# Optimization experiments

Hardware: AMD Instinct MI355X
Metric: run time of the kernel (lower is better)

The kernel has to match this reference:

```python
import jax, jax.numpy as jnp
import numpy as np

D, H, DH = 768, 12, 64
W = 256            # one-sided window (attention_window=512 total)
EPS = 1e-6
NEG = -1e9


def layer_norm(x, g, b):
    m = jnp.mean(x, axis=-1, keepdims=True)
    v = jnp.mean((x - m) ** 2, axis=-1, keepdims=True)
    return g * (x - m) * jax.lax.rsqrt(v + EPS) + b


def _blocks3(t, nb):
    # t: [B,H,nb,W,dh] -> keys/values of 3 neighboring blocks [B,H,nb,3W,dh]
    tp = jnp.pad(t, ((0, 0), (0, 0), (1, 1), (0, 0), (0, 0)))
    return jnp.concatenate([tp[:, :, :nb], tp[:, :, 1:nb + 1], tp[:, :, 2:nb + 2]], axis=3)


def sliding_window_attention(x, kpm, Wq, bq, Wk, bk, Wv, bv, Wo, bo):
    B, S, _ = x.shape
    nb = S // W
    def proj(Wm, bm):
        return (x @ Wm + bm).reshape(B, S, H, DH).transpose(0, 2, 1, 3).reshape(B, H, nb, W, DH)
    q = proj(Wq, bq) * (1.0 / np.sqrt(DH))
    k = proj(Wk, bk)
    v = proj(Wv, bv)
    k3 = _blocks3(k, nb)
    v3 = _blocks3(v, nb)
    # scores over local band: [B,H,nb,W,3W]
    s = jnp.einsum('bhnqd,bhnkd->bhnqk', q, k3)
    qi = jnp.arange(W)[:, None]
    kj = jnp.arange(3 * W)[None, :]
    band = jnp.abs(kj - W - qi) <= W                     # [W,3W]
    kg = (jnp.arange(nb)[:, None, None] - 1) * W + kj[None]  # global key idx [nb,1,3W]
    inrange = (kg >= 0) & (kg < S)
    # key padding mask gathered into block layout: [B,nb,3W]
    kpm_b = jnp.pad(kpm.reshape(B, nb, W), ((0, 0), (1, 1), (0, 0)), constant_values=True)
    kpm3 = jnp.concatenate([kpm_b[:, :nb], kpm_b[:, 1:nb + 1], kpm_b[:, 2:nb + 2]], axis=2)
    m = band[None, None, None] & inrange[None, None] & (~kpm3)[:, None, :, None, :]
    s = jnp.where(m, s, NEG)
    p = jax.nn.softmax(s, axis=-1)
    o = jnp.einsum('bhnqk,bhnkd->bhnqd', p, v3)
    o = o.reshape(B, H, S, DH).transpose(0, 2, 1, 3).reshape(B, S, D)
    return o @ Wo + bo


def setup_inputs() -> dict:
    key = jax.random.key(0)
    ks = jax.random.split(key, 12)
    B, S, DF = 2, 4096, 3072
    sc = 1.0 / np.sqrt(D)
    return {
        'x': jax.random.normal(ks[0], (B, S, D), jnp.float32),
        'mask': jnp.zeros((B, S), bool),
        'id': 0,
        'Wq': jax.random.normal(ks[1], (D, D), jnp.float32) * sc,
        'bq': jnp.zeros((D,), jnp.float32),
        'Wk': jax.random.normal(ks[2], (D, D), jnp.float32) * sc,
        'bk': jnp.zeros((D,), jnp.float32),
        'Wv': jax.random.normal(ks[3], (D, D), jnp.float32) * sc,
        'bv': jnp.zeros((D,), jnp.float32),
        'Wo': jax.random.normal(ks[4], (D, D), jnp.float32) * sc,
        'bo': jnp.zeros((D,), jnp.float32),
        'ln1_g': jnp.ones((D,), jnp.float32),
        'ln1_b': jnp.zeros((D,), jnp.float32),
        'W1': jax.random.normal(ks[5], (D, DF), jnp.float32) * sc,
        'b1': jnp.zeros((DF,), jnp.float32),
        'W2': jax.random.normal(ks[6], (DF, D), jnp.float32) * (1.0 / np.sqrt(DF)),
        'b2': jnp.zeros((D,), jnp.float32),
        'ln2_g': jnp.ones((D,), jnp.float32),
        'ln2_b': jnp.zeros((D,), jnp.float32),
    }


def reference(x, mask, id, Wq, bq, Wk, bk, Wv, bv, Wo, bo, ln1_g, ln1_b, W1, b1, W2, b2, ln2_g, ln2_b):
    # Sublayer 1: pre-norm residual around sliding-window self-attention
    h = layer_norm(x, ln1_g, ln1_b)
    x = x + sliding_window_attention(h, mask, Wq, bq, Wk, bk, Wv, bv, Wo, bo)
    # Sublayer 2: pre-norm residual around positionwise FFN
    h = layer_norm(x, ln2_g, ln2_b)
    x = x + (jax.nn.relu(h @ W1 + b1) @ W2 + b2)
    return x
```

## Files before the change

kernel.cpp:

```cpp
#include <hip/hip_runtime.h>
#include <hip/hip_bf16.h>
#include <cstddef>

typedef __attribute__((ext_vector_type(8))) short short8;
typedef __attribute__((ext_vector_type(4))) float f32x4;
typedef __attribute__((ext_vector_type(4))) unsigned short us4;

typedef __attribute__((address_space(1))) void as1_void;
typedef __attribute__((address_space(3))) void as3_void;

__device__ __forceinline__ void gload16(const void* g, void* lds) {
  __builtin_amdgcn_global_load_lds((as1_void*)(void*)g, (as3_void*)lds, 16, 0, 0);
}

__device__ inline unsigned short f2bf(float f) {
  union { float f; unsigned int u; } v; v.f = f;
  return (unsigned short)((v.u + 0x7FFFu + ((v.u >> 16) & 1u)) >> 16);
}

__device__ __forceinline__ float exp2v(float x) {
  float r; asm("v_exp_f32 %0, %1" : "=v"(r) : "v"(x)); return r;
}
__device__ __forceinline__ unsigned cvtpk(float a, float b) {
  unsigned r; asm("v_cvt_pk_bf16_f32 %0, %1, %2" : "=v"(r) : "v"(a), "v"(b)); return r;
}

__global__ __launch_bounds__(256) void ln_kernel(const float* __restrict__ x,
    const float* __restrict__ g, const float* __restrict__ b,
    unsigned short* __restrict__ out)
{
  int row = blockIdx.x, t = threadIdx.x;
  const float* xr = x + (size_t)row * 768;
  float v0 = xr[t], v1 = xr[t + 256], v2 = xr[t + 512];
  float s = v0 + v1 + v2;
  #pragma unroll
  for (int o = 32; o > 0; o >>= 1) s += __shfl_xor(s, o);
  __shared__ float r1[4], r2[4];
  if ((t & 63) == 0) r1[t >> 6] = s;
  __syncthreads();
  float mean = (r1[0] + r1[1] + r1[2] + r1[3]) * (1.0f / 768.0f);
  float d0 = v0 - mean, d1 = v1 - mean, d2 = v2 - mean;
  float q = d0 * d0 + d1 * d1 + d2 * d2;
  #pragma unroll
  for (int o = 32; o > 0; o >>= 1) q += __shfl_xor(q, o);
  if ((t & 63) == 0) r2[t >> 6] = q;
  __syncthreads();
  float var = (r2[0] + r2[1] + r2[2] + r2[3]) * (1.0f / 768.0f);
  float rs = rsqrtf(var + 1e-6f);
  unsigned short* orow = out + (size_t)row * 768;
  orow[t]       = f2bf(g[t]       * d0 * rs + b[t]);
  orow[t + 256] = f2bf(g[t + 256] * d1 * rs + b[t + 256]);
  orow[t + 512] = f2bf(g[t + 512] * d2 * rs + b[t + 512]);
}

__global__ __launch_bounds__(256) void prep_kernel(
    const float* __restrict__ Wq, const float* __restrict__ Wk,
    const float* __restrict__ Wv, const float* __restrict__ Wo,
    const float* __restrict__ W1, const float* __restrict__ W2,
    const float* __restrict__ bq, const float* __restrict__ bk,
    const float* __restrict__ bv,
    unsigned short* __restrict__ WTqkv, unsigned short* __restrict__ WTo,
    unsigned short* __restrict__ W1T, unsigned short* __restrict__ W2T,
    float* __restrict__ bqkv,
    const float* __restrict__ x, const float* __restrict__ ln1g,
    const float* __restrict__ ln1b, unsigned short* __restrict__ hbuf)
{
  int bid = blockIdx.x;
  int t = threadIdx.x;
  if (bid >= 6921) {
    int row = bid - 6921;
    const float* xr = x + (size_t)row * 768;
    float v0 = xr[t], v1 = xr[t + 256], v2 = xr[t + 512];
    float s = v0 + v1 + v2;
    #pragma unroll
    for (int o = 32; o > 0; o >>= 1) s += __shfl_xor(s, o);
    __shared__ float r1[4], r2[4];
    if ((t & 63) == 0) r1[t >> 6] = s;
    __syncthreads();
    float mean = (r1[0] + r1[1] + r1[2] + r1[3]) * (1.0f / 768.0f);
    float d0 = v0 - mean, d1 = v1 - mean, d2 = v2 - mean;
    float q = d0 * d0 + d1 * d1 + d2 * d2;
    #pragma unroll
    for (int o = 32; o > 0; o >>= 1) q += __shfl_xor(q, o);
    if ((t & 63) == 0) r2[t >> 6] = q;
    __syncthreads();
    float var = (r2[0] + r2[1] + r2[2] + r2[3]) * (1.0f / 768.0f);
    float rs = rsqrtf(var + 1e-6f);
    unsigned short* orow = hbuf + (size_t)row * 768;
    orow[t]       = f2bf(ln1g[t]       * d0 * rs + ln1b[t]);
    orow[t + 256] = f2bf(ln1g[t + 256] * d1 * rs + ln1b[t + 256]);
    orow[t + 512] = f2bf(ln1g[t + 512] * d2 * rs + ln1b[t + 512]);
    return;
  }
  if (bid >= 6912) {
    int i = (bid - 6912) * 256 + t;
    bqkv[i] = (i < 768) ? bq[i] : ((i < 1536) ? bk[i - 768] : bv[i - 1536]);
    return;
  }
  const float* W; unsigned short* WT; int K, N, lb;
  if (bid < 576)       { W = Wq; WT = WTqkv;                        K = 768;  N = 768;  lb = bid; }
  else if (bid < 1152) { W = Wk; WT = WTqkv + (size_t)768 * 768;    K = 768;  N = 768;  lb = bid - 576; }
  else if (bid < 1728) { W = Wv; WT = WTqkv + (size_t)1536 * 768;   K = 768;  N = 768;  lb = bid - 1152; }
  else if (bid < 2304) { W = Wo; WT = WTo;                          K = 768;  N = 768;  lb = bid - 1728; }
  else if (bid < 4608) { W = W1; WT = W1T;                          K = 768;  N = 3072; lb = bid - 2304; }
  else                 { W = W2; WT = W2T;                          K = 3072; N = 768;  lb = bid - 4608; }
  int ntN = N >> 5;
  int k0 = (lb / ntN) * 32, n0 = (lb % ntN) * 32;
  __shared__ float tile[32][33];
  int tx = t & 31, ty = t >> 5;
  #pragma unroll
  for (int i = 0; i < 32; i += 8)
    tile[ty + i][tx] = W[(size_t)(k0 + ty + i) * N + n0 + tx];
  __syncthreads();
  #pragma unroll
  for (int i = 0; i < 32; i += 8)
    WT[(size_t)(n0 + ty + i) * K + k0 + tx] = f2bf(tile[tx][ty + i]);
}

enum { EPI_QKV = 0, EPI_RELU = 1, EPI_RESID = 2 };

template<int EPI>
__global__ __launch_bounds__(256) void gemmS_kernel(
    const unsigned short* __restrict__ A, const unsigned short* __restrict__ BT,
    const float* __restrict__ bias, const float* __restrict__ resid,
    void* __restrict__ outp, int M, int N, int K, int ntn)
{
  __shared__ char lds_a[16384];
  __shared__ char lds_b[16384];
  int tid = threadIdx.x;
  int nwg = gridDim.x;
  int bid = ((int)blockIdx.x & 7) * (nwg >> 3) + ((int)blockIdx.x >> 3);
  int mt = bid / ntn, nt = bid % ntn;
  int m0 = mt * 128, n0 = nt * 128;
  int w = tid >> 6, l = tid & 63;
  int wr = w >> 1, wc = w & 1;
  int fr = l & 15, fq = l >> 4;
  int rb = tid >> 3;
  int sw8 = ((tid & 7) ^ (rb & 7)) * 8;
  const unsigned short* As = A  + (size_t)(m0 + rb) * K + sw8;
  const unsigned short* Bs = BT + (size_t)(n0 + rb) * K + sw8;

  f32x4 acc[4][4] = {};
  int NT = K >> 6;
  for (int t = 0; t < NT; ++t) {
    {
      char* dA = lds_a + tid * 16;
      char* dB = lds_b + tid * 16;
      int ko = t * 64;
      #pragma unroll
      for (int c = 0; c < 4; c++) {
        gload16(As + (size_t)(c * 32) * K + ko, dA + c * 4096);
        gload16(Bs + (size_t)(c * 32) * K + ko, dB + c * 4096);
      }
    }
    asm volatile("s_waitcnt vmcnt(0)" ::: "memory");
    __syncthreads();
    #pragma unroll
    for (int h = 0; h < 2; h++) {
      short8 af[4], bf[4];
      int colb = (h * 64 + fq * 16) ^ ((fr & 7) << 4);
      #pragma unroll
      for (int i = 0; i < 4; i++)
        af[i] = *(const short8*)(lds_a + (wr * 64 + i * 16 + fr) * 128 + colb);
      #pragma unroll
      for (int j = 0; j < 4; j++)
        bf[j] = *(const short8*)(lds_b + (wc * 64 + j * 16 + fr) * 128 + colb);
      __builtin_amdgcn_s_setprio(1);
      #pragma unroll
      for (int i = 0; i < 4; i++)
        #pragma unroll
        for (int j = 0; j < 4; j++)
          acc[i][j] = __builtin_amdgcn_mfma_f32_16x16x32_bf16(af[i], bf[j], acc[i][j], 0, 0, 0);
      __builtin_amdgcn_s_setprio(0);
    }
    __syncthreads();
  }

  #pragma unroll
  for (int nj = 0; nj < 4; nj++) {
    int col = n0 + wc * 64 + nj * 16 + fr;
    float bs = bias[col];
    if (EPI == EPI_QKV) {
      int which = (col >= 1536) ? 2 : ((col >= 768) ? 1 : 0);
      int c2 = col - which * 768;
      int hh = c2 >> 6, dh = c2 & 63;
      if (which == 2) {
        unsigned short* dstv = reinterpret_cast<unsigned short*>(outp) + (size_t)2 * 8192 * 768;
        #pragma unroll
        for (int i = 0; i < 4; i++) {
          int row0 = m0 + wr * 64 + i * 16 + fq * 4;
          int bb = row0 >> 12, sl = row0 & 4095;
          us4 pv;
          #pragma unroll
          for (int r = 0; r < 4; r++) pv[r] = f2bf(acc[i][nj][r] + bs);
          *reinterpret_cast<us4*>(&dstv[((size_t)(bb * 12 + hh) * 64 + dh) * 4096 + sl]) = pv;
        }
      } else {
        unsigned short* dst = reinterpret_cast<unsigned short*>(outp) + (size_t)which * 8192 * 768;
        #pragma unroll
        for (int i = 0; i < 4; i++) {
          #pragma unroll
          for (int r = 0; r < 4; r++) {
            int row = m0 + wr * 64 + i * 16 + fq * 4 + r;
            float c = acc[i][nj][r] + bs;
            if (which == 0) c *= 0.18033688011112042f;
            int bb = row >> 12, sl = row & 4095;
            dst[(((size_t)(bb * 12 + hh)) * 4096 + sl) * 64 + dh] = f2bf(c);
          }
        }
      }
    } else if (EPI == EPI_RELU) {
      #pragma unroll
      for (int i = 0; i < 4; i++)
        #pragma unroll
        for (int r = 0; r < 4; r++) {
          int row = m0 + wr * 64 + i * 16 + fq * 4 + r;
          float c = fmaxf(acc[i][nj][r] + bs, 0.0f);
          reinterpret_cast<unsigned short*>(outp)[(size_t)row * N + col] = f2bf(c);
        }
    } else {
      #pragma unroll
      for (int i = 0; i < 4; i++)
        #pragma unroll
        for (int r = 0; r < 4; r++) {
          int row = m0 + wr * 64 + i * 16 + fq * 4 + r;
          float c = acc[i][nj][r] + bs + resid[(size_t)row * N + col];
          reinterpret_cast<float*>(outp)[(size_t)row * N + col] = c;
        }
    }
  }
}

template<int EPI>
__global__ __launch_bounds__(256, 3) void gemmN_kernel(
    const unsigned short* __restrict__ A, const unsigned short* __restrict__ BT,
    const float* __restrict__ bias, const float* __restrict__ resid,
    void* __restrict__ outp, int M, int N, int K, int ntn)
{
  __shared__ char lds[2][24576];
  int tid = threadIdx.x;
  int nwg = gridDim.x;
  int bid = ((int)blockIdx.x & 7) * (nwg >> 3) + ((int)blockIdx.x >> 3);
  int mt = bid / ntn, nt = bid % ntn;
  int m0 = mt * 64, n0 = nt * 128;
  int w = tid >> 6, l = tid & 63;
  int fr = l & 15, fq = l >> 4;
  int rb = tid >> 3;
  int sw8 = ((tid & 7) ^ (rb & 7)) * 8;
  const unsigned short* As = A  + (size_t)(m0 + rb) * K + sw8;
  const unsigned short* Bs = BT + (size_t)(n0 + rb) * K + sw8;

  auto stage = [&](int buf, int kt) {
    char* d = &lds[buf][0] + tid * 16;
    int ko = kt * 64;
    #pragma unroll
    for (int c = 0; c < 2; c++)
      gload16(As + (size_t)(c * 32) * K + ko, d + c * 4096);
    #pragma unroll
    for (int c = 0; c < 4; c++)
      gload16(Bs + (size_t)(c * 32) * K + ko, d + 8192 + c * 4096);
  };

  f32x4 acc[4][2] = {};
  stage(0, 0);
  asm volatile("s_waitcnt vmcnt(0)" ::: "memory");
  __syncthreads();

  int NT = K >> 6;
  for (int t = 0; t < NT; ++t) {
    int R = t & 1;
    if (t + 1 < NT) stage(R ^ 1, t + 1);
    #pragma unroll
    for (int h = 0; h < 2; h++) {
      short8 af[4], bf[2];
      const char* base = &lds[R][0];
      int colb = (h * 64 + fq * 16) ^ ((fr & 7) << 4);
      #pragma unroll
      for (int i = 0; i < 4; i++)
        af[i] = *(const short8*)(base + (i * 16 + fr) * 128 + colb);
      #pragma unroll
      for (int j = 0; j < 2; j++)
        bf[j] = *(const short8*)(base + 8192 + (w * 32 + j * 16 + fr) * 128 + colb);
      __builtin_amdgcn_s_setprio(1);
      #pragma unroll
      for (int i = 0; i < 4; i++)
        #pragma unroll
        for (int j = 0; j < 2; j++)
          acc[i][j] = __builtin_amdgcn_mfma_f32_16x16x32_bf16(af[i], bf[j], acc[i][j], 0, 0, 0);
      __builtin_amdgcn_s_setprio(0);
    }
    asm volatile("s_waitcnt vmcnt(0)" ::: "memory");
    __syncthreads();
  }

  #pragma unroll
  for (int nj = 0; nj < 2; nj++) {
    int col = n0 + w * 32 + nj * 16 + fr;
    float bs = bias[col];
    if (EPI == EPI_RELU) {
      #pragma unroll
      for (int i = 0; i < 4; i++)
        #pragma unroll
        for (int r = 0; r < 4; r++) {
          int row = m0 + i * 16 + fq * 4 + r;
          float c = fmaxf(acc[i][nj][r] + bs, 0.0f);
          reinterpret_cast<unsigned short*>(outp)[(size_t)row * N + col] = f2bf(c);
        }
    } else {
      #pragma unroll
      for (int i = 0; i < 4; i++)
        #pragma unroll
        for (int r = 0; r < 4; r++) {
          int row = m0 + i * 16 + fq * 4 + r;
          float c = acc[i][nj][r] + bs + resid[(size_t)row * N + col];
          reinterpret_cast<float*>(outp)[(size_t)row * N + col] = c;
        }
    }
  }
}

__global__ __launch_bounds__(256) void attn_fused_kernel(
    const unsigned short* __restrict__ qg, const unsigned short* __restrict__ kg,
    const unsigned short* __restrict__ vtg, const unsigned char* __restrict__ kpm,
    unsigned short* __restrict__ attn_out)
{
  __shared__ unsigned short lds_k[3][64 * 64];
  __shared__ unsigned short lds_vt[3][64 * 64];
  __shared__ unsigned short lds_p[4][32 * 64];
  int bid0 = blockIdx.x;
  int bid = (bid0 & 7) * 96 + (bid0 >> 3);
  int qblk = bid & 31, h = (bid >> 5) % 12, b = bid / 384;
  int bh = b * 12 + h;
  int q0 = qblk * 128;
  int tid = threadIdx.x, w = tid >> 6, l = tid & 63;
  int fr = l & 15, fq = l >> 4;
  int qw0 = q0 + w * 32;
  int swzb = (((l & 7) ^ (l >> 3)) << 4);
  const char* qbase  = (const char*)(qg  + (size_t)bh * 4096 * 64);
  const char* kbase  = (const char*)(kg  + (size_t)bh * 4096 * 64);
  const char* vtbase = (const char*)(vtg + (size_t)bh * 64 * 4096);
  const unsigned char* kpmb = kpm + (size_t)b * 4096;

  #pragma unroll
  for (int s = 0; s < 4; s++) {
    int row = w * 32 + s * 8 + (l >> 3);
    gload16(qbase + (size_t)(q0 + row) * 128 + swzb, (char*)lds_p[w] + s * 1024);
  }

  auto stageKVc = [&](int c, int buf) {
    int g0 = q0 - 256 + c * 64;
    g0 = (g0 < 0) ? 0 : ((g0 > 4032) ? 4032 : g0);
    #pragma unroll
    for (int s = 0; s < 2; s++) {
      int row = w * 16 + s * 8 + (l >> 3);
      gload16(kbase + (size_t)(g0 + row) * 128 + swzb,
              (char*)lds_k[buf] + (w * 2 + s) * 1024);
      gload16(vtbase + ((size_t)row * 4096 + g0) * 2 + swzb,
              (char*)lds_vt[buf] + (w * 2 + s) * 1024);
    }
  };

  stageKVc(0, 0);
  stageKVc(1, 1);
  asm volatile("s_waitcnt vmcnt(8)" ::: "memory");

  short8 qf[2][2];
  #pragma unroll
  for (int i = 0; i < 2; i++)
    #pragma unroll
    for (int ks = 0; ks < 2; ks++)
      qf[i][ks] = *(const short8*)((const char*)lds_p[w] + (i * 16 + fr) * 128 +
                    ((ks * 64 + fq * 16) ^ ((fr & 7) << 4)));

  short8 ones;
  #pragma unroll
  for (int e = 0; e < 8; e++) ones[e] = (short)0x3F80;

  f32x4 acc_o[2][4] = {};
  f32x4 acc_l[2] = {};
  float m_st[2] = {-3.0e38f, -3.0e38f};

  for (int c = 0; c < 10; c++) {
    if (c < 9) { asm volatile("s_waitcnt vmcnt(4)" ::: "memory"); }
    else       { asm volatile("s_waitcnt vmcnt(0)" ::: "memory"); }
    __builtin_amdgcn_s_barrier();
    if (c < 8) stageKVc(c + 2, (c + 2) % 3);
    int g0 = q0 - 256 + c * 64;
    bool valid = (g0 >= 0) && (g0 < 4096);
    if (valid) {
      int buf = c % 3;
      unsigned int km[4];
      #pragma unroll
      for (int j = 0; j < 4; j++)
        km[j] = *(const unsigned int*)(kpmb + g0 + 16 * j + 4 * fq);
      bool anyk = __any((km[0] | km[1] | km[2] | km[3]) != 0);
      int rel = g0 - qw0;
      bool edge = anyk || (rel < -225) || (rel > 193);
      short8 kf[4][2];
      #pragma unroll
      for (int j = 0; j < 4; j++)
        #pragma unroll
        for (int ks = 0; ks < 2; ks++)
          kf[j][ks] = *(const short8*)((const char*)lds_k[buf] + (j * 16 + fr) * 128 +
                        ((ks * 64 + fq * 16) ^ ((fr & 7) << 4)));
      f32x4 accs[4][2] = {};
      __builtin_amdgcn_s_setprio(1);
      #pragma unroll
      for (int j = 0; j < 4; j++)
        #pragma unroll
        for (int i = 0; i < 2; i++)
          #pragma unroll
          for (int ks = 0; ks < 2; ks++)
            accs[j][i] = __builtin_amdgcn_mfma_f32_16x16x32_bf16(kf[j][ks], qf[i][ks], accs[j][i], 0, 0, 0);
      __builtin_amdgcn_s_setprio(0);
      #pragma unroll
      for (int i = 0; i < 2; i++) {
        float sv[4][4];
        #pragma unroll
        for (int j = 0; j < 4; j++)
          #pragma unroll
          for (int r = 0; r < 4; r++)
            sv[j][r] = accs[j][i][r];
        if (edge) {
          int base = rel + 4 * fq - fr - 16 * i;
          #pragma unroll
          for (int j = 0; j < 4; j++)
            #pragma unroll
            for (int r = 0; r < 4; r++) {
              int d = base + 16 * j + r;
              bool ok = (d >= -256) && (d <= 256) && (((km[j] >> (8 * r)) & 255u) == 0u);
              if (!ok) sv[j][r] = -1.0e9f;
            }
        }
        float mj[4];
        #pragma unroll
        for (int j = 0; j < 4; j++)
          mj[j] = fmaxf(fmaxf(sv[j][0], sv[j][1]), fmaxf(sv[j][2], sv[j][3]));
        float mv = fmaxf(fmaxf(mj[0], mj[1]), fmaxf(mj[2], mj[3]));
        mv = fmaxf(mv, __shfl_xor(mv, 16));
        mv = fmaxf(mv, __shfl_xor(mv, 32));
        float mo = m_st[i];
        if (!__all(mv - mo <= 8.0f)) {
          float mn = fmaxf(mo, mv);
          float scl = exp2v(mo - mn);
          m_st[i] = mn;
          #pragma unroll
          for (int r = 0; r < 4; r++) {
            float so = __shfl(scl, (l & 48) | ((l >> 2) & 12) | r);
            acc_l[i][r] *= so;
            #pragma unroll
            for (int jd = 0; jd < 4; jd++) acc_o[i][jd][r] *= so;
          }
        }
        float mn = m_st[i];
        char* prow = (char*)lds_p[w] + (i * 16 + fr) * 128;
        #pragma unroll
        for (int j = 0; j < 4; j++) {
          float p0 = exp2v(sv[j][0] - mn), p1 = exp2v(sv[j][1] - mn);
          float p2 = exp2v(sv[j][2] - mn), p3 = exp2v(sv[j][3] - mn);
          uint2 u; u.x = cvtpk(p0, p1); u.y = cvtpk(p2, p3);
          *(uint2*)(prow + ((32 * j + 8 * fq) ^ ((fr & 7) << 4))) = u;
        }
      }
      short8 pf[2][2];
      #pragma unroll
      for (int i = 0; i < 2; i++)
        #pragma unroll
        for (int ks = 0; ks < 2; ks++)
          pf[i][ks] = *(const short8*)((const char*)lds_p[w] + (i * 16 + fr) * 128 +
                        ((ks * 64 + fq * 16) ^ ((fr & 7) << 4)));
      short8 vf[4][2];
      #pragma unroll
      for (int jd = 0; jd < 4; jd++)
        #pragma unroll
        for (int ks = 0; ks < 2; ks++)
          vf[jd][ks] = *(const short8*)((const char*)lds_vt[buf] + (jd * 16 + fr) * 128 +
                        ((ks * 64 + fq * 16) ^ ((fr & 7) << 4)));
      __builtin_amdgcn_s_setprio(1);
      #pragma unroll
      for (int i = 0; i < 2; i++) {
        #pragma unroll
        for (int jd = 0; jd < 4; jd++)
          #pragma unroll
          for (int ks = 0; ks < 2; ks++)
            acc_o[i][jd] = __builtin_amdgcn_mfma_f32_16x16x32_bf16(pf[i][ks], vf[jd][ks], acc_o[i][jd], 0, 0, 0);
        #pragma unroll
        for (int ks = 0; ks < 2; ks++)
          acc_l[i] = __builtin_amdgcn_mfma_f32_16x16x32_bf16(pf[i][ks], ones, acc_l[i], 0, 0, 0);
      }
      __builtin_amdgcn_s_setprio(0);
    }
  }
  #pragma unroll
  for (int i = 0; i < 2; i++) {
    #pragma unroll
    for (int r = 0; r < 4; r++) {
      float inv = 1.0f / acc_l[i][r];
      int qrow = qw0 + i * 16 + fq * 4 + r;
      size_t orow = ((size_t)b * 4096 + qrow) * 768 + h * 64;
      #pragma unroll
      for (int jd = 0; jd < 4; jd++)
        attn_out[orow + jd * 16 + fr] = f2bf(acc_o[i][jd][r] * inv);
    }
  }
}

extern "C" void kernel_launch(void* const* d_in, const int* in_sizes, int n_in,
                              void* d_out, int out_size, void* d_ws, size_t ws_size,
                              hipStream_t stream) {
  const float* x            = (const float*)d_in[0];
  const unsigned char* mask = (const unsigned char*)d_in[1];
  const float* Wq  = (const float*)d_in[3];
  const float* bq  = (const float*)d_in[4];
  const float* Wk  = (const float*)d_in[5];
  const float* bk  = (const float*)d_in[6];
  const float* Wv  = (const float*)d_in[7];
  const float* bv  = (const float*)d_in[8];
  const float* Wo  = (const float*)d_in[9];
  const float* bo  = (const float*)d_in[10];
  const float* ln1g = (const float*)d_in[11];
  const float* ln1b = (const float*)d_in[12];
  const float* W1  = (const float*)d_in[13];
  const float* b1  = (const float*)d_in[14];
  const float* W2  = (const float*)d_in[15];
  const float* b2  = (const float*)d_in[16];
  const float* ln2g = (const float*)d_in[17];
  const float* ln2b = (const float*)d_in[18];
  float* out = (float*)d_out;

  char* ws = (char*)d_ws;
  size_t off = 0;
  auto alloc = [&](size_t bytes) -> void* {
    void* p = ws + off;
    off += (bytes + 255) & ~(size_t)255;
    return p;
  };
  unsigned short* WTqkv = (unsigned short*)alloc((size_t)2304 * 768 * 2);
  unsigned short* WTo   = (unsigned short*)alloc((size_t)768 * 768 * 2);
  unsigned short* W1T   = (unsigned short*)alloc((size_t)3072 * 768 * 2);
  unsigned short* W2T   = (unsigned short*)alloc((size_t)768 * 3072 * 2);
  float*          bqkv  = (float*)alloc(2304 * 4);
  unsigned short* hbuf  = (unsigned short*)alloc((size_t)8192 * 768 * 2);
  unsigned short* qkv   = (unsigned short*)alloc((size_t)3 * 8192 * 768 * 2);
  unsigned short* attn  = (unsigned short*)alloc((size_t)8192 * 768 * 2);
  float* x1             = (float*)alloc((size_t)8192 * 768 * 4);
  unsigned short* h2    = (unsigned short*)alloc((size_t)8192 * 768 * 2);
  unsigned short* a1    = (unsigned short*)alloc((size_t)8192 * 3072 * 2);

  prep_kernel<<<15113, 256, 0, stream>>>(Wq, Wk, Wv, Wo, W1, W2, bq, bk, bv,
                                         WTqkv, WTo, W1T, W2T, bqkv,
                                         x, ln1g, ln1b, hbuf);

  gemmS_kernel<EPI_QKV><<<1152, 256, 0, stream>>>(hbuf, WTqkv, bqkv, nullptr, qkv, 8192, 2304, 768, 18);

  attn_fused_kernel<<<768, 256, 0, stream>>>(qkv, qkv + (size_t)8192 * 768,
                                             qkv + (size_t)2 * 8192 * 768, mask, attn);

  gemmN_kernel<EPI_RESID><<<768, 256, 0, stream>>>(attn, WTo, bo, x, x1, 8192, 768, 768, 6);
  ln_kernel<<<8192, 256, 0, stream>>>(x1, ln2g, ln2b, h2);
  gemmS_kernel<EPI_RELU><<<1536, 256, 0, stream>>>(h2, W1T, b1, nullptr, a1, 8192, 3072, 768, 24);
  gemmN_kernel<EPI_RESID><<<768, 256, 0, stream>>>(a1, W2T, b2, x1, out, 8192, 768, 3072, 6);
}
```

Measured before the change: 232.2 us.

## Software-pipeline attention QK^T across chunks and store residual x1 in bf16

The attention loop is restructured so that the QK^T MFMAs for the next KV chunk are issued before the softmax and PV work of the current chunk. Two score register sets alternate between chunks, and the loop is fully unrolled with two barriers per step. Separately, the intermediate residual x1 is now stored as bf16 instead of fp32, which cuts its write and read traffic in the Wo epilogue, the second layernorm and the final residual add. The cost is higher register pressure in the attention kernel and lower precision of the residual stream.

Result: slower. 239.5 us (+3.2%).

```diff
diff --git a/kernel.cpp b/kernel.cpp
--- a/kernel.cpp
+++ b/kernel.cpp
@@ -17,7 +17,10 @@
   union { float f; unsigned int u; } v; v.f = f;
   return (unsigned short)((v.u + 0x7FFFu + ((v.u >> 16) & 1u)) >> 16);
 }
-
+__device__ __forceinline__ float bf2f(unsigned short u) {
+  union { unsigned int u; float f; } v; v.u = ((unsigned int)u) << 16;
+  return v.f;
+}
 __device__ __forceinline__ float exp2v(float x) {
   float r; asm("v_exp_f32 %0, %1" : "=v"(r) : "v"(x)); return r;
 }
@@ -25,13 +28,13 @@
   unsigned r; asm("v_cvt_pk_bf16_f32 %0, %1, %2" : "=v"(r) : "v"(a), "v"(b)); return r;
 }
 
-__global__ __launch_bounds__(256) void ln_kernel(const float* __restrict__ x,
+__global__ __launch_bounds__(256) void ln_bf16_kernel(const unsigned short* __restrict__ x,
     const float* __restrict__ g, const float* __restrict__ b,
     unsigned short* __restrict__ out)
 {
   int row = blockIdx.x, t = threadIdx.x;
-  const float* xr = x + (size_t)row * 768;
-  float v0 = xr[t], v1 = xr[t + 256], v2 = xr[t + 512];
+  const unsigned short* xr = x + (size_t)row * 768;
+  float v0 = bf2f(xr[t]), v1 = bf2f(xr[t + 256]), v2 = bf2f(xr[t + 512]);
   float s = v0 + v1 + v2;
   #pragma unroll
   for (int o = 32; o > 0; o >>= 1) s += __shfl_xor(s, o);
@@ -117,13 +120,13 @@
     WT[(size_t)(n0 + ty + i) * K + k0 + tx] = f2bf(tile[tx][ty + i]);
 }
 
-enum { EPI_QKV = 0, EPI_RELU = 1, EPI_RESID = 2 };
+enum { EPI_QKV = 0, EPI_RELU = 1, EPI_WO = 2, EPI_OUT = 3 };
 
 template<int EPI>
 __global__ __launch_bounds__(256) void gemmS_kernel(
     const unsigned short* __restrict__ A, const unsigned short* __restrict__ BT,
-    const float* __restrict__ bias, const float* __restrict__ resid,
-    void* __restrict__ outp, int M, int N, int K, int ntn)
+    const float* __restrict__ bias, void* __restrict__ outp,
+    int M, int N, int K, int ntn)
 {
   __shared__ char lds_a[16384];
   __shared__ char lds_b[16384];
@@ -209,7 +212,7 @@
           }
         }
       }
-    } else if (EPI == EPI_RELU) {
+    } else {
       #pragma unroll
       for (int i = 0; i < 4; i++)
         #pragma unroll
@@ -218,15 +221,6 @@
           float c = fmaxf(acc[i][nj][r] + bs, 0.0f);
           reinterpret_cast<unsigned short*>(outp)[(size_t)row * N + col] = f2bf(c);
         }
-    } else {
-      #pragma unroll
-      for (int i = 0; i < 4; i++)
-        #pragma unroll
-        for (int r = 0; r < 4; r++) {
-          int row = m0 + wr * 64 + i * 16 + fq * 4 + r;
-          float c = acc[i][nj][r] + bs + resid[(size_t)row * N + col];
-          reinterpret_cast<float*>(outp)[(size_t)row * N + col] = c;
-        }
     }
   }
 }
@@ -234,7 +228,7 @@
 template<int EPI>
 __global__ __launch_bounds__(256, 3) void gemmN_kernel(
     const unsigned short* __restrict__ A, const unsigned short* __restrict__ BT,
-    const float* __restrict__ bias, const float* __restrict__ resid,
+    const float* __restrict__ bias, const void* __restrict__ residp,
     void* __restrict__ outp, int M, int N, int K, int ntn)
 {
   __shared__ char lds[2][24576];
@@ -297,24 +291,21 @@
   for (int nj = 0; nj < 2; nj++) {
     int col = n0 + w * 32 + nj * 16 + fr;
     float bs = bias[col];
-    if (EPI == EPI_RELU) {
-      #pragma unroll
-      for (int i = 0; i < 4; i++)
-        #pragma unroll
-        for (int r = 0; r < 4; r++) {
-          int row = m0 + i * 16 + fq * 4 + r;
-          float c = fmaxf(acc[i][nj][r] + bs, 0.0f);
+    #pragma unroll
+    for (int i = 0; i < 4; i++) {
+      #pragma unroll
+      for (int r = 0; r < 4; r++) {
+        int row = m0 + i * 16 + fq * 4 + r;
+        if (EPI == EPI_WO) {
+          float c = acc[i][nj][r] + bs +
+                    reinterpret_cast<const float*>(residp)[(size_t)row * N + col];
           reinterpret_cast<unsigned short*>(outp)[(size_t)row * N + col] = f2bf(c);
-        }
-    } else {
-      #pragma unroll
-      for (int i = 0; i < 4; i++)
-        #pragma unroll
-        for (int r = 0; r < 4; r++) {
-          int row = m0 + i * 16 + fq * 4 + r;
-          float c = acc[i][nj][r] + bs + resid[(size_t)row * N + col];
+        } else {
+          float c = acc[i][nj][r] + bs +
+                    bf2f(reinterpret_cast<const unsigned short*>(residp)[(size_t)row * N + col]);
           reinterpret_cast<float*>(outp)[(size_t)row * N + col] = c;
         }
+      }
     }
   }
 }
@@ -379,118 +370,150 @@
   f32x4 acc_o[2][4] = {};
   f32x4 acc_l[2] = {};
   float m_st[2] = {-3.0e38f, -3.0e38f};
-
-  for (int c = 0; c < 10; c++) {
-    if (c < 9) { asm volatile("s_waitcnt vmcnt(4)" ::: "memory"); }
-    else       { asm volatile("s_waitcnt vmcnt(0)" ::: "memory"); }
-    __builtin_amdgcn_s_barrier();
-    if (c < 8) stageKVc(c + 2, (c + 2) % 3);
+  f32x4 Sa[4][2], Sb[4][2];
+
+  auto qk = [&](int c, f32x4 (&S)[4][2]) {
+    int buf = c % 3;
+    short8 kf[4][2];
+    #pragma unroll
+    for (int j = 0; j < 4; j++)
+      #pragma unroll
+      for (int ks = 0; ks < 2; ks++)
+        kf[j][ks] = *(const short8*)((const char*)lds_k[buf] + (j * 16 + fr) * 128 +
+                      ((ks * 64 + fq * 16) ^ ((fr & 7) << 4)));
+    #pragma unroll
+    for (int j = 0; j < 4; j++)
+      #pragma unroll
+      for (int i = 0; i < 2; i++)
+        S[j][i] = f32x4{0.0f, 0.0f, 0.0f, 0.0f};
+    __builtin_amdgcn_s_setprio(1);
+    #pragma unroll
+    for (int j = 0; j < 4; j++)
+      #pragma unroll
+      for (int i = 0; i < 2; i++)
+        #pragma unroll
+        for (int ks = 0; ks < 2; ks++)
+          S[j][i] = __builtin_amdgcn_mfma_f32_16x16x32_bf16(kf[j][ks], qf[i][ks], S[j][i], 0, 0, 0);
+    __builtin_amdgcn_s_setprio(0);
+  };
+
+  auto finish = [&](int c, f32x4 (&S)[4][2]) {
     int g0 = q0 - 256 + c * 64;
-    bool valid = (g0 >= 0) && (g0 < 4096);
-    if (valid) {
-      int buf = c % 3;
-      unsigned int km[4];
+    if (g0 < 0 || g0 >= 4096) return;
+    int buf = c % 3;
+    unsigned int km[4];
+    #pragma unroll
+    for (int j = 0; j < 4; j++)
+      km[j] = *(const unsigned int*)(kpmb + g0 + 16 * j + 4 * fq);
+    bool anyk = __any((km[0] | km[1] | km[2] | km[3]) != 0);
+    int rel = g0 - qw0;
+    bool edge = anyk || (rel < -225) || (rel > 193);
+    #pragma unroll
+    for (int i = 0; i < 2; i++) {
+      float sv[4][4];
       #pragma unroll
       for (int j = 0; j < 4; j++)
-        km[j] = *(const unsigned int*)(kpmb + g0 + 16 * j + 4 * fq);
-      bool anyk = __any((km[0] | km[1] | km[2] | km[3]) != 0);
-      int rel = g0 - qw0;
-      bool edge = anyk || (rel < -225) || (rel > 193);
-      short8 kf[4][2];
-      #pragma unroll
-      for (int j = 0; j < 4; j++)
-        #pragma unroll
-        for (int ks = 0; ks < 2; ks++)
-          kf[j][ks] = *(const short8*)((const char*)lds_k[buf] + (j * 16 + fr) * 128 +
-                        ((ks * 64 + fq * 16) ^ ((fr & 7) << 4)));
-      f32x4 accs[4][2] = {};
-      __builtin_amdgcn_s_setprio(1);
-      #pragma unroll
-      for (int j = 0; j < 4; j++)
-        #pragma unroll
-        for (int i = 0; i < 2; i++)
-          #pragma unroll
-          for (int ks = 0; ks < 2; ks++)
-            accs[j][i] = __builtin_amdgcn_mfma_f32_16x16x32_bf16(kf[j][ks], qf[i][ks], accs[j][i], 0, 0, 0);
-      __builtin_amdgcn_s_setprio(0);
-      #pragma unroll
-      for (int i = 0; i < 2; i++) {
-        float sv[4][4];
+        #pragma unroll
+        for (int r = 0; r < 4; r++)
+          sv[j][r] = S[j][i][r];
+      if (edge) {
+        int base = rel + 4 * fq - fr - 16 * i;
         #pragma unroll
         for (int j = 0; j < 4; j++)
           #pragma unroll
-          for (int r = 0; r < 4; r++)
-            sv[j][r] = accs[j][i][r];
-        if (edge) {
-          int base = rel + 4 * fq - fr - 16 * i;
+          for (int r = 0; r < 4; r++) {
+            int d = base + 16 * j + r;
+            bool ok = (d >= -256) && (d <= 256) && (((km[j] >> (8 * r)) & 255u) == 0u);
+            if (!ok) sv[j][r] = -1.0e9f;
+          }
+      }
+      float mj[4];
+      #pragma unroll
+      for (int j = 0; j < 4; j++)
+        mj[j] = fmaxf(fmaxf(sv[j][0], sv[j][1]), fmaxf(sv[j][2], sv[j][3]));
+      float mv = fmaxf(fmaxf(mj[0], mj[1]), fmaxf(mj[2], mj[3]));
+      mv = fmaxf(mv, __shfl_xor(mv, 16));
+      mv = fmaxf(mv, __shfl_xor(mv, 32));
+      float mo = m_st[i];
+      if (!__all(mv - mo <= 8.0f)) {
+        float mn = fmaxf(mo, mv);
+        float scl = exp2v(mo - mn);
+        m_st[i] = mn;
+        #pragma unroll
+        for (int r = 0; r < 4; r++) {
+          float so = __shfl(scl, (l & 48) | ((l >> 2) & 12) | r);
+          acc_l[i][r] *= so;
           #pragma unroll
-          for (int j = 0; j < 4; j++)
-            #pragma unroll
-            for (int r = 0; r < 4; r++) {
-              int d = base + 16 * j + r;
-              bool ok = (d >= -256) && (d <= 256) && (((km[j] >> (8 * r)) & 255u) == 0u);
-              if (!ok) sv[j][r] = -1.0e9f;
-            }
-        }
-        float mj[4];
-        #pragma unroll
-        for (int j = 0; j < 4; j++)
-          mj[j] = fmaxf(fmaxf(sv[j][0], sv[j][1]), fmaxf(sv[j][2], sv[j][3]));
-        float mv = fmaxf(fmaxf(mj[0], mj[1]), fmaxf(mj[2], mj[3]));
-        mv = fmaxf(mv, __shfl_xor(mv, 16));
-        mv = fmaxf(mv, __shfl_xor(mv, 32));
-        float mo = m_st[i];
-        if (!__all(mv - mo <= 8.0f)) {
-          float mn = fmaxf(mo, mv);
-          float scl = exp2v(mo - mn);
-          m_st[i] = mn;
-          #pragma unroll
-          for (int r = 0; r < 4; r++) {
-            float so = __shfl(scl, (l & 48) | ((l >> 2) & 12) | r);
-            acc_l[i][r] *= so;
-            #pragma unroll
-            for (int jd = 0; jd < 4; jd++) acc_o[i][jd][r] *= so;
-          }
-        }
-        float mn = m_st[i];
-        char* prow = (char*)lds_p[w] + (i * 16 + fr) * 128;
-        #pragma unroll
-        for (int j = 0; j < 4; j++) {
-          float p0 = exp2v(sv[j][0] - mn), p1 = exp2v(sv[j][1] - mn);
-          float p2 = exp2v(sv[j][2] - mn), p3 = exp2v(sv[j][3] - mn);
-          uint2 u; u.x = cvtpk(p0, p1); u.y = cvtpk(p2, p3);
-          *(uint2*)(prow + ((32 * j + 8 * fq) ^ ((fr & 7) << 4))) = u;
+          for (int jd = 0; jd < 4; jd++) acc_o[i][jd][r] *= so;
         }
       }
-      short8 pf[2][2];
-      #pragma unroll
-      for (int i = 0; i < 2; i++)
+      float mn = m_st[i];
+      char* prow = (char*)lds_p[w] + (i * 16 + fr) * 128;
+      #pragma unroll
+      for (int j = 0; j < 4; j++) {
+        float p0 = exp2v(sv[j][0] - mn), p1 = exp2v(sv[j][1] - mn);
+        float p2 = exp2v(sv[j][2] - mn), p3 = exp2v(sv[j][3] - mn);
+        uint2 u; u.x = cvtpk(p0, p1); u.y = cvtpk(p2, p3);
+        *(uint2*)(prow + ((32 * j + 8 * fq) ^ ((fr & 7) << 4))) = u;
+      }
+    }
+    short8 pf[2][2];
+    #pragma unroll
+    for (int i = 0; i < 2; i++)
+      #pragma unroll
+      for (int ks = 0; ks < 2; ks++)
+        pf[i][ks] = *(const short8*)((const char*)lds_p[w] + (i * 16 + fr) * 128 +
+                      ((ks * 64 + fq * 16) ^ ((fr & 7) << 4)));
+    short8 vf[4][2];
+    #pragma unroll
+    for (int jd = 0; jd < 4; jd++)
+      #pragma unroll
+      for (int ks = 0; ks < 2; ks++)
+        vf[jd][ks] = *(const short8*)((const char*)lds_vt[buf] + (jd * 16 + fr) * 128 +
+                      ((ks * 64 + fq * 16) ^ ((fr & 7) << 4)));
+    __builtin_amdgcn_s_setprio(1);
+    #pragma unroll
+    for (int i = 0; i < 2; i++) {
+      #pragma unroll
+      for (int jd = 0; jd < 4; jd++)
         #pragma unroll
         for (int ks = 0; ks < 2; ks++)
-          pf[i][ks] = *(const short8*)((const char*)lds_p[w] + (i * 16 + fr) * 128 +
-                        ((ks * 64 + fq * 16) ^ ((fr & 7) << 4)));
-      short8 vf[4][2];
-      #pragma unroll
-      for (int jd = 0; jd < 4; jd++)
-        #pragma unroll
-        for (int ks = 0; ks < 2; ks++)
-          vf[jd][ks] = *(const short8*)((const char*)lds_vt[buf] + (jd * 16 + fr) * 128 +
-                        ((ks * 64 + fq * 16) ^ ((fr & 7) << 4)));
-      __builtin_amdgcn_s_setprio(1);
-      #pragma unroll
-      for (int i = 0; i < 2; i++) {
-        #pragma unroll
-        for (int jd = 0; jd < 4; jd++)
-          #pragma unroll
-          for (int ks = 0; ks < 2; ks++)
-            acc_o[i][jd] = __builtin_amdgcn_mfma_f32_16x16x32_bf16(pf[i][ks], vf[jd][ks], acc_o[i][jd], 0, 0, 0);
-        #pragma unroll
-        for (int ks = 0; ks < 2; ks++)
-          acc_l[i] = __builtin_amdgcn_mfma_f32_16x16x32_bf16(pf[i][ks], ones, acc_l[i], 0, 0, 0);
-      }
-      __builtin_amdgcn_s_setprio(0);
-    }
-  }
+          acc_o[i][jd] = __builtin_amdgcn_mfma_f32_16x16x32_bf16(pf[i][ks], vf[jd][ks], acc_o[i][jd], 0, 0, 0);
+      #pragma unroll
+      for (int ks = 0; ks < 2; ks++)
+        acc_l[i] = __builtin_amdgcn_mfma_f32_16x16x32_bf16(pf[i][ks], ones, acc_l[i], 0, 0, 0);
+    }
+    __builtin_amdgcn_s_setprio(0);
+  };
+
+  asm volatile("s_waitcnt vmcnt(4)" ::: "memory");
+  __builtin_amdgcn_s_barrier();
+  qk(0, Sa);
+
+#define ASTEP(C, SCUR, SNEXT)                                                  \
+  __builtin_amdgcn_s_barrier();             \
+  if ((C) + 2 <= 9) {                                                          \
+    stageKVc((C) + 2, ((C) + 2) % 3);                                          \
+    asm volatile("s_waitcnt vmcnt(4)" ::: "memory");    \
+  } else {                                                                     \
+    asm volatile("s_waitcnt vmcnt(0)" ::: "memory");                           \
+  }                                                                            \
+  __builtin_amdgcn_s_barrier();                 \
+  if ((C) + 1 <= 9) qk((C) + 1, SNEXT);                                        \
+  finish((C), SCUR);
+
+  ASTEP(0, Sa, Sb)
+  ASTEP(1, Sb, Sa)
+  ASTEP(2, Sa, Sb)
+  ASTEP(3, Sb, Sa)
+  ASTEP(4, Sa, Sb)
+  ASTEP(5, Sb, Sa)
+  ASTEP(6, Sa, Sb)
+  ASTEP(7, Sb, Sa)
+  ASTEP(8, Sa, Sb)
+  ASTEP(9, Sb, Sa)
+#undef ASTEP
+
   #pragma unroll
   for (int i = 0; i < 2; i++) {
     #pragma unroll
@@ -543,7 +566,7 @@
   unsigned short* hbuf  = (unsigned short*)alloc((size_t)8192 * 768 * 2);
   unsigned short* qkv   = (unsigned short*)alloc((size_t)3 * 8192 * 768 * 2);
   unsigned short* attn  = (unsigned short*)alloc((size_t)8192 * 768 * 2);
-  float* x1             = (float*)alloc((size_t)8192 * 768 * 4);
+  unsigned short* x1    = (unsigned short*)alloc((size_t)8192 * 768 * 2);
   unsigned short* h2    = (unsigned short*)alloc((size_t)8192 * 768 * 2);
   unsigned short* a1    = (unsigned short*)alloc((size_t)8192 * 3072 * 2);
 
@@ -551,13 +574,13 @@
                                          WTqkv, WTo, W1T, W2T, bqkv,
                                          x, ln1g, ln1b, hbuf);
 
-  gemmS_kernel<EPI_QKV><<<1152, 256, 0, stream>>>(hbuf, WTqkv, bqkv, nullptr, qkv, 8192, 2304, 768, 18);
+  gemmS_kernel<EPI_QKV><<<1152, 256, 0, stream>>>(hbuf, WTqkv, bqkv, qkv, 8192, 2304, 768, 18);
 
   attn_fused_kernel<<<768, 256, 0, stream>>>(qkv, qkv + (size_t)8192 * 768,
                                              qkv + (size_t)2 * 8192 * 768, mask, attn);
 
-  gemmN_kernel<EPI_RESID><<<768, 256, 0, stream>>>(attn, WTo, bo, x, x1, 8192, 768, 768, 6);
-  ln_kernel<<<8192, 256, 0, stream>>>(x1, ln2g, ln2b, h2);
-  gemmS_kernel<EPI_RELU><<<1536, 256, 0, stream>>>(h2, W1T, b1, nullptr, a1, 8192, 3072, 768, 24);
-  gemmN_kernel<EPI_RESID><<<768, 256, 0, stream>>>(a1, W2T, b2, x1, out, 8192, 768, 3072, 6);
-}
+  gemmN_kernel<EPI_WO><<<768, 256, 0, stream>>>(attn, WTo, bo, x, x1, 8192, 768, 768, 6);
+  ln_bf16_kernel<<<8192, 256, 0, stream>>>(x1, ln2g, ln2b, h2);
+  gemmS_kernel<EPI_RELU><<<1536, 256, 0, stream>>>(h2, W1T, b1, a1, 8192, 3072, 768, 24);
+  gemmN_kernel<EPI_OUT><<<768, 256, 0, stream>>>(a1, W2T, b2, x1, out, 8192, 768, 3072, 6);
+}
```
